# Kernel tuning notes

Measured on AMD Instinct MI355X. Metric: run time of the kernel, lower is better.

## Reference

```python
import jax, jax.numpy as jnp
import numpy as np

EMBED, HEADS, LEVELS, POINTS, CAMS, ZANCH = 256, 8, 4, 8, 6, 4
HEAD_DIM = EMBED // HEADS
NQ, BS = 10000, 1
SHAPES = np.array([[92, 160], [46, 80], [23, 40], [12, 20]], dtype=np.int64)
NV = int((SHAPES[:, 0] * SHAPES[:, 1]).sum())  # 19560


def setup_inputs() -> dict:
    key = jax.random.key(0)
    ks = jax.random.split(key, 10)
    f = lambda k, s, sc=1.0: jax.random.normal(k, s, dtype=jnp.float32) * sc
    lsi = np.concatenate([[0], np.cumsum(SHAPES[:, 0] * SHAPES[:, 1])[:-1]]).astype(np.int64)
    return dict(
        query=f(ks[0], (BS, NQ, EMBED)),
        query_pos=f(ks[1], (BS, NQ, EMBED)),
        value=f(ks[2], (CAMS, NV, BS, EMBED)),
        reference_points=jax.random.uniform(ks[3], (CAMS, BS, NQ, ZANCH, 2), dtype=jnp.float32),
        bev_mask=jax.random.bernoulli(ks[4], 0.3, (CAMS, BS, NQ, ZANCH)),
        spatial_shapes=jnp.asarray(SHAPES),
        level_start_index=jnp.asarray(lsi),
        Wv=f(ks[5], (EMBED, EMBED), 0.02), bv=jnp.zeros((EMBED,), jnp.float32),
        Woff=f(ks[6], (EMBED, HEADS * LEVELS * POINTS * 2), 0.02),
        boff=f(ks[7], (HEADS * LEVELS * POINTS * 2,), 0.5),
        Watt=f(ks[8], (EMBED, HEADS * LEVELS * POINTS), 0.02),
        batt=jnp.zeros((HEADS * LEVELS * POINTS,), jnp.float32),
        Wout=f(ks[9], (EMBED, EMBED), 0.02), bout=jnp.zeros((EMBED,), jnp.float32),
    )


def _bilinear_gather(v2, x, y, H, W):
    # v2: (BH, H*W, hd); x, y: (BH, N) pixel coords. grid_sample bilinear,
    # align_corners=False, padding_mode='zeros' semantics.
    x0 = jnp.floor(x); y0 = jnp.floor(y)
    lx = x - x0; ly = y - y0
    x0i = x0.astype(jnp.int32); y0i = y0.astype(jnp.int32)
    out = jnp.zeros(x.shape + (v2.shape[-1],), v2.dtype)
    for dx, dy, w in ((0, 0, (1 - lx) * (1 - ly)), (1, 0, lx * (1 - ly)),
                      (0, 1, (1 - lx) * ly), (1, 1, lx * ly)):
        xi = x0i + dx; yi = y0i + dy
        valid = (xi >= 0) & (xi < W) & (yi >= 0) & (yi < H)
        idx = jnp.clip(yi, 0, H - 1) * W + jnp.clip(xi, 0, W - 1)
        g = jnp.take_along_axis(v2, idx[..., None], axis=1)
        out = out + g * (w * valid.astype(v2.dtype))[..., None]
    return out


def _ms_deform_attn(q, v, ref, shapes, lsi, Wv, bv, Woff, boff, Watt, batt):
    # q: (B, nq, C); v: (B, nv, C); ref: (B, nq, D, 2)
    B, nq, C = q.shape
    v = (v @ Wv + bv).reshape(B, -1, HEADS, HEAD_DIM)
    off = (q @ Woff + boff).reshape(B, nq, HEADS, LEVELS, POINTS, 2)
    attw = jax.nn.softmax((q @ Watt + batt).reshape(B, nq, HEADS, LEVELS * POINTS), axis=-1)
    attw = attw.reshape(B, nq, HEADS, LEVELS, POINTS)
    # offset normalizer: (w_l, h_l) per level
    norm = jnp.asarray(np.stack([shapes[:, 1], shapes[:, 0]], -1), q.dtype)  # (L, 2)
    off = off / norm[None, None, None, :, None, :]
    off = off.reshape(B, nq, HEADS, LEVELS, POINTS // ZANCH, ZANCH, 2)
    loc = (ref[:, :, None, None, None] + off).reshape(B, nq, HEADS, LEVELS, POINTS, 2)
    acc = jnp.zeros((B, HEADS, nq, HEAD_DIM), q.dtype)
    for l in range(LEVELS):
        H, W = int(shapes[l, 0]), int(shapes[l, 1])
        s = int(lsi[l])
        vl = v[:, s:s + H * W].transpose(0, 2, 1, 3).reshape(B * HEADS, H * W, HEAD_DIM)
        ll = loc[:, :, :, l].transpose(0, 2, 1, 3, 4).reshape(B * HEADS, nq * POINTS, 2)
        x = ll[..., 0] * W - 0.5
        y = ll[..., 1] * H - 0.5
        samp = _bilinear_gather(vl, x, y, H, W).reshape(B, HEADS, nq, POINTS, HEAD_DIM)
        w = attw[:, :, :, l].transpose(0, 2, 1, 3)  # (B, HEADS, nq, POINTS)
        acc = acc + (samp * w[..., None]).sum(3)
    return acc.transpose(0, 2, 1, 3).reshape(B, nq, C)


def reference(query, query_pos, value, reference_points, bev_mask, spatial_shapes,
              level_start_index, Wv, bv, Woff, boff, Watt, batt, Wout, bout):
    shapes = np.asarray(spatial_shapes)
    lsi = np.asarray(level_start_index)
    B, nq, C = query.shape
    cams = value.shape[0]
    q = query + query_pos
    # replicate queries per camera (equivalent to rebatch-by-mask: unselected
    # outputs are masked out before accumulation)
    q_cam = jnp.broadcast_to(q[:, None], (B, cams, nq, C)).reshape(B * cams, nq, C)
    v = value.transpose(2, 0, 1, 3).reshape(B * cams, -1, C)
    ref = reference_points.transpose(1, 0, 2, 3, 4).reshape(B * cams, nq, ZANCH, 2)
    out = _ms_deform_attn(q_cam, v, ref, shapes, lsi, Wv, bv, Woff, boff, Watt, batt)
    out = out.reshape(B, cams, nq, C)
    # query selection per camera uses batch 0 of bev_mask, as in the original
    m = (bev_mask[:, 0].sum(-1) > 0)  # (cams, nq)
    slots = (out * m[None, :, :, None].astype(out.dtype)).sum(1)  # (B, nq, C)
    count = (bev_mask.sum(-1) > 0).astype(query.dtype).transpose(1, 2, 0).sum(-1)
    count = jnp.maximum(count, 1.0)  # (B, nq)
    slots = slots / count[..., None]
    # dropout in eval mode is identity
    return slots @ Wout + bout + query
```

## Files before the change

### kernel.cpp

```cpp
#include <hip/hip_runtime.h>
#include <hip/hip_bf16.h>

constexpr int NQ = 10000, NV = 19560, CAMS = 6, EMBED = 256, HEADS = 8,
              HEAD_DIM = 32, LEVELS = 4, POINTS = 8;
constexpr int MQ_PAD = 10112;
constexpr int MV_PAD = 117376;

typedef unsigned int u32;
typedef unsigned short u16;
typedef unsigned char u8;
typedef __attribute__((ext_vector_type(8))) short short8v;
typedef __attribute__((ext_vector_type(4))) float f32x4;
typedef __attribute__((ext_vector_type(2))) float f32x2;

__device__ inline u16 f2bf(float f) {
  __hip_bfloat16 b = __float2bfloat16(f);
  return *(u16*)&b;
}

__global__ void conv_bf16_kernel(const float* __restrict__ a, const float* __restrict__ b,
                                 u16* __restrict__ dst, int M, int Mpad) {
  int i = blockIdx.x * blockDim.x + threadIdx.x;
  if (i >= Mpad * 32) return;
  int row = i >> 5;
  int col = (i & 31) * 8;
  u16 o[8];
  if (row < M) {
    const float* pa = a + (size_t)row * 256 + col;
#pragma unroll
    for (int j = 0; j < 8; ++j) {
      float v = pa[j];
      if (b) v += b[(size_t)row * 256 + col + j];
      o[j] = f2bf(v);
    }
  } else {
#pragma unroll
    for (int j = 0; j < 8; ++j) o[j] = 0;
  }
  *(short8v*)&dst[(size_t)row * 256 + col] = *(short8v*)o;
}

__global__ void transpose_w_kernel(const float* __restrict__ src, u16* __restrict__ dst, int N) {
  int g = blockIdx.x * blockDim.x + threadIdx.x;
  if (g >= N * 256) return;
  int n = g >> 8, k = g & 255;
  dst[(size_t)n * 256 + k] = f2bf(src[(size_t)k * N + n]);
}

__global__ void catbias_kernel(const float* __restrict__ boff, const float* __restrict__ batt,
                               float* __restrict__ catb) {
  int i = blockIdx.x * blockDim.x + threadIdx.x;
  if (i < 512) catb[i] = boff[i];
  else if (i < 768) catb[i] = batt[i - 512];
}

__global__ void mask_kernel(const int* __restrict__ bev, unsigned char* __restrict__ m,
                            float* __restrict__ cinv) {
  int q = blockIdx.x * blockDim.x + threadIdx.x;
  if (q >= NQ) return;
  int cnt = 0;
  for (int c = 0; c < CAMS; ++c) {
    int any = 0;
    for (int z = 0; z < 4; ++z) any |= bev[((size_t)c * NQ + q) * 4 + z];
    m[c * NQ + q] = (unsigned char)(any != 0);
    cnt += (any != 0);
  }
  cinv[q] = 1.0f / (float)(cnt > 0 ? cnt : 1);
}

__global__ __launch_bounds__(256) void gemm_mfma(
    const u16* __restrict__ A, const u16* __restrict__ Bt,
    const float* __restrict__ bias, const float* __restrict__ add,
    void* __restrict__ Cout, void* __restrict__ Cout2, int M, int N, int mode) {
  constexpr int K = 256, BK = 64;
  __shared__ u16 As[128 * BK];
  __shared__ u16 Bs[128 * BK];
  const int tid = threadIdx.x;
  const int lane = tid & 63, w = tid >> 6;
  const int wr = w >> 1, wc = w & 1;
  const int row0 = blockIdx.y * 128, col0 = blockIdx.x * 128;
  f32x4 acc[4][4] = {};

  for (int k0 = 0; k0 < K; k0 += BK) {
    short8v areg[4], breg[4];
#pragma unroll
    for (int j = 0; j < 4; ++j) {
      int e = tid + j * 256;
      int r = e >> 3, cb = (e & 7) * 16;
      areg[j] = *(const short8v*)((const char*)A + ((size_t)(row0 + r) * K + k0) * 2 + cb);
      breg[j] = *(const short8v*)((const char*)Bt + ((size_t)(col0 + r) * K + k0) * 2 + cb);
    }
    __syncthreads();
#pragma unroll
    for (int j = 0; j < 4; ++j) {
      int e = tid + j * 256;
      int r = e >> 3, cb = (e & 7) * 16;
      int sw = cb ^ ((r & 7) << 4);
      *(short8v*)((char*)As + r * 128 + sw) = areg[j];
      *(short8v*)((char*)Bs + r * 128 + sw) = breg[j];
    }
    __syncthreads();
#pragma unroll
    for (int kk = 0; kk < 2; ++kk) {
      short8v af[4], bf[4];
#pragma unroll
      for (int m = 0; m < 4; ++m) {
        int r = wr * 64 + m * 16 + (lane & 15);
        int cb = kk * 64 + (lane >> 4) * 16;
        af[m] = *(const short8v*)((const char*)As + r * 128 + (cb ^ ((r & 7) << 4)));
      }
#pragma unroll
      for (int n = 0; n < 4; ++n) {
        int r = wc * 64 + n * 16 + (lane & 15);
        int cb = kk * 64 + (lane >> 4) * 16;
        bf[n] = *(const short8v*)((const char*)Bs + r * 128 + (cb ^ ((r & 7) << 4)));
      }
#pragma unroll
      for (int m = 0; m < 4; ++m)
#pragma unroll
        for (int n = 0; n < 4; ++n)
          acc[m][n] = __builtin_amdgcn_mfma_f32_16x16x32_bf16(af[m], bf[n], acc[m][n], 0, 0, 0);
    }
  }

#pragma unroll
  for (int m = 0; m < 4; ++m) {
    int rowb = row0 + wr * 64 + m * 16 + (lane >> 4) * 4;
#pragma unroll
    for (int r = 0; r < 4; ++r) {
      int rr = rowb + r;
      if (rr >= M) continue;
#pragma unroll
      for (int n = 0; n < 4; ++n) {
        int col = col0 + wc * 64 + n * 16 + (lane & 15);
        float v = acc[m][n][r] + bias[col];
        if (mode == 0) {
          ((float*)Cout)[(size_t)rr * N + col] = v;
        } else if (mode == 2) {
          ((float*)Cout)[(size_t)rr * N + col] = v + add[(size_t)rr * N + col];
        } else {
          if (col < 512) ((float*)Cout)[(size_t)rr * 512 + col] = v;
          else           ((float*)Cout2)[(size_t)rr * 256 + (col - 512)] = v;
        }
      }
    }
  }
}

__global__ __launch_bounds__(256) void gemm_wv_f32(
    const float* __restrict__ A, const u16* __restrict__ Bt,
    const float* __restrict__ bias, u8* __restrict__ Cout, int M) {
  constexpr int K = 256, BK = 64, N = 256;
  __shared__ u16 As[128 * BK];
  __shared__ u16 Bs[128 * BK];
  const int tid = threadIdx.x;
  const int lane = tid & 63, w = tid >> 6;
  const int wr = w >> 1, wc = w & 1;
  const int row0 = blockIdx.y * 128, col0 = blockIdx.x * 128;
  f32x4 acc[4][4] = {};

  for (int k0 = 0; k0 < K; k0 += BK) {
    short8v areg[4], breg[4];
#pragma unroll
    for (int j = 0; j < 4; ++j) {
      int e = tid + j * 256;
      int r = e >> 3, co = (e & 7) * 8;
      u16 tmp[8];
      if (row0 + r < M) {
        const float* src = A + (size_t)(row0 + r) * K + k0 + co;
        float4 f0 = *(const float4*)src;
        float4 f1 = *(const float4*)(src + 4);
        tmp[0] = f2bf(f0.x); tmp[1] = f2bf(f0.y); tmp[2] = f2bf(f0.z); tmp[3] = f2bf(f0.w);
        tmp[4] = f2bf(f1.x); tmp[5] = f2bf(f1.y); tmp[6] = f2bf(f1.z); tmp[7] = f2bf(f1.w);
      } else {
#pragma unroll
        for (int t = 0; t < 8; ++t) tmp[t] = 0;
      }
      areg[j] = *(short8v*)tmp;
      breg[j] = *(const short8v*)((const char*)Bt + ((size_t)(col0 + r) * K + k0) * 2 + co * 2);
    }
    __syncthreads();
#pragma unroll
    for (int j = 0; j < 4; ++j) {
      int e = tid + j * 256;
      int r = e >> 3, cb = (e & 7) * 16;
      int sw = cb ^ ((r & 7) << 4);
      *(short8v*)((char*)As + r * 128 + sw) = areg[j];
      *(short8v*)((char*)Bs + r * 128 + sw) = breg[j];
    }
    __syncthreads();
#pragma unroll
    for (int kk = 0; kk < 2; ++kk) {
      short8v af[4], bf[4];
#pragma unroll
      for (int m = 0; m < 4; ++m) {
        int r = wr * 64 + m * 16 + (lane & 15);
        int cb = kk * 64 + (lane >> 4) * 16;
        af[m] = *(const short8v*)((const char*)As + r * 128 + (cb ^ ((r & 7) << 4)));
      }
#pragma unroll
      for (int n = 0; n < 4; ++n) {
        int r = wc * 64 + n * 16 + (lane & 15);
        int cb = kk * 64 + (lane >> 4) * 16;
        bf[n] = *(const short8v*)((const char*)Bs + r * 128 + (cb ^ ((r & 7) << 4)));
      }
#pragma unroll
      for (int m = 0; m < 4; ++m)
#pragma unroll
        for (int n = 0; n < 4; ++n)
          acc[m][n] = __builtin_amdgcn_mfma_f32_16x16x32_bf16(af[m], bf[n], acc[m][n], 0, 0, 0);
    }
  }

#pragma unroll
  for (int m = 0; m < 4; ++m) {
    int rowb = row0 + wr * 64 + m * 16 + (lane >> 4) * 4;
#pragma unroll
    for (int r = 0; r < 4; ++r) {
      int rr = rowb + r;
      if (rr >= M) continue;
      int cam = rr / NV;
      int px = rr - cam * NV;
#pragma unroll
      for (int n = 0; n < 4; ++n) {
        int col = col0 + wc * 64 + n * 16 + (lane & 15);
        float v = acc[m][n][r] + bias[col];
        int h = col >> 5, d = col & 31;
        int pk = __builtin_amdgcn_cvt_pk_fp8_f32(v, v, 0, false);
        Cout[(((size_t)cam * HEADS + h) * NV + px) * 32 + d] = (u8)(pk & 0xff);
      }
    }
  }
}

__global__ void softmax_kernel(float* __restrict__ att) {
  int r = blockIdx.x * blockDim.x + threadIdx.x;
  if (r >= NQ * HEADS) return;
  float* p = att + (size_t)r * 32;
  float mx = -1e30f;
#pragma unroll
  for (int i = 0; i < 32; ++i) mx = fmaxf(mx, p[i]);
  float e[32], sm = 0.f;
#pragma unroll
  for (int i = 0; i < 32; ++i) { e[i] = expf(p[i] - mx); sm += e[i]; }
  float inv = 1.0f / sm;
#pragma unroll
  for (int i = 0; i < 32; ++i) p[i] = e[i] * inv;
}

__global__ __launch_bounds__(256, 8) void sample_kernel(
    const u8* __restrict__ vproj, const float* __restrict__ offr,
    const float* __restrict__ attw, const float* __restrict__ ref,
    const unsigned char* __restrict__ m, float* __restrict__ part) {
  constexpr int Hs[4] = {92, 46, 23, 12};
  constexpr int Ws[4] = {160, 80, 40, 20};
  constexpr int LSI[4] = {0, 14720, 18400, 19320};
  const int c = blockIdx.y;
  const int q = blockIdx.x * 4 + (threadIdx.x >> 6);
  if (!m[c * NQ + q]) return;
  const int lane = threadIdx.x & 63;
  const int h = lane >> 3;
  const int pp = (lane >> 2) & 1;
  const int d0 = (lane & 3) * 8;

  float acc[8] = {};
  const float* refc = ref + ((size_t)c * NQ + q) * 8;
  float rfx[4], rfy[4];
#pragma unroll
  for (int z = 0; z < 4; ++z) { rfx[z] = refc[z * 2]; rfy[z] = refc[z * 2 + 1]; }
  const float* offq = offr + (size_t)q * 512 + h * 64;
  const float* attq = attw + (size_t)q * 256 + h * 32;
  const u8* vch = vproj + ((size_t)c * HEADS + h) * NV * 32 + d0;

#pragma unroll
  for (int l = 0; l < LEVELS; ++l) {
    const int W = Ws[l], H = Hs[l];
    const u8* vl = vch + (size_t)LSI[l] * 32;
#pragma unroll 2
    for (int pi = 0; pi < 4; ++pi) {
      const int p = pi * 2 + pp;
      const int z = p & 3;
      float2 o = *(const float2*)&offq[l * 16 + p * 2];
      float x = rfx[z] * (float)W + o.x - 0.5f;
      float y = rfy[z] * (float)H + o.y - 0.5f;
      float x0f = floorf(x), y0f = floorf(y);
      float lx = x - x0f, ly = y - y0f;
      int x0 = (int)x0f, y0 = (int)y0f;
      float fx0 = (x0 >= 0 && x0 < W) ? 1.f : 0.f;
      float fx1 = (x0 >= -1 && x0 < W - 1) ? 1.f : 0.f;
      float fy0 = (y0 >= 0 && y0 < H) ? 1.f : 0.f;
      float fy1 = (y0 >= -1 && y0 < H - 1) ? 1.f : 0.f;
      int x0c = min(max(x0, 0), W - 1);
      int x1c = min(max(x0 + 1, 0), W - 1);
      int y0c = min(max(y0, 0), H - 1);
      int y1c = min(max(y0 + 1, 0), H - 1);
      uint2 v00 = *(const uint2*)(vl + (size_t)(y0c * W + x0c) * 32);
      uint2 v01 = *(const uint2*)(vl + (size_t)(y0c * W + x1c) * 32);
      uint2 v10 = *(const uint2*)(vl + (size_t)(y1c * W + x0c) * 32);
      uint2 v11 = *(const uint2*)(vl + (size_t)(y1c * W + x1c) * 32);
      float a = attq[l * 8 + p];
      float c00 = a * (1.f - lx) * (1.f - ly) * fx0 * fy0;
      float c01 = a * lx * (1.f - ly) * fx1 * fy0;
      float c10 = a * (1.f - lx) * ly * fx0 * fy1;
      float c11 = a * lx * ly * fx1 * fy1;
#pragma unroll
      for (int half = 0; half < 2; ++half) {
        u32 w00 = half ? v00.y : v00.x, w01 = half ? v01.y : v01.x;
        u32 w10 = half ? v10.y : v10.x, w11 = half ? v11.y : v11.x;
        f32x2 gA0 = __builtin_amdgcn_cvt_pk_f32_fp8(w00, false);
        f32x2 gA1 = __builtin_amdgcn_cvt_pk_f32_fp8(w00, true);
        f32x2 gB0 = __builtin_amdgcn_cvt_pk_f32_fp8(w01, false);
        f32x2 gB1 = __builtin_amdgcn_cvt_pk_f32_fp8(w01, true);
        f32x2 gC0 = __builtin_amdgcn_cvt_pk_f32_fp8(w10, false);
        f32x2 gC1 = __builtin_amdgcn_cvt_pk_f32_fp8(w10, true);
        f32x2 gD0 = __builtin_amdgcn_cvt_pk_f32_fp8(w11, false);
        f32x2 gD1 = __builtin_amdgcn_cvt_pk_f32_fp8(w11, true);
        int b = half * 4;
        acc[b + 0] += c00 * gA0.x + c01 * gB0.x + c10 * gC0.x + c11 * gD0.x;
        acc[b + 1] += c00 * gA0.y + c01 * gB0.y + c10 * gC0.y + c11 * gD0.y;
        acc[b + 2] += c00 * gA1.x + c01 * gB1.x + c10 * gC1.x + c11 * gD1.x;
        acc[b + 3] += c00 * gA1.y + c01 * gB1.y + c10 * gC1.y + c11 * gD1.y;
      }
    }
  }
#pragma unroll
  for (int d = 0; d < 8; ++d) acc[d] += __shfl_xor(acc[d], 4);
  if (pp == 0) {
    float* sp = part + ((size_t)c * NQ + q) * EMBED + h * 32 + d0;
    f32x4 v0 = {acc[0], acc[1], acc[2], acc[3]};
    f32x4 v1 = {acc[4], acc[5], acc[6], acc[7]};
    __builtin_nontemporal_store(v0, (f32x4*)sp);
    __builtin_nontemporal_store(v1, (f32x4*)(sp + 4));
  }
}

__global__ void reduce_kernel(const float* __restrict__ part, const unsigned char* __restrict__ m,
                              const float* __restrict__ cinv, u16* __restrict__ sbf) {
  int i = blockIdx.x * blockDim.x + threadIdx.x;
  if (i >= MQ_PAD * 32) return;
  int row = i >> 5;
  int col = (i & 31) * 8;
  u16 o[8];
  if (row < NQ) {
    float s[8] = {};
    for (int c = 0; c < CAMS; ++c) {
      if (!m[c * NQ + row]) continue;
      const f32x4* pp = (const f32x4*)(part + ((size_t)c * NQ + row) * EMBED + col);
      f32x4 f0 = __builtin_nontemporal_load(pp);
      f32x4 f1 = __builtin_nontemporal_load(pp + 1);
#pragma unroll
      for (int j = 0; j < 4; ++j) { s[j] += f0[j]; s[4 + j] += f1[j]; }
    }
    float sc = cinv[row];
#pragma unroll
    for (int j = 0; j < 8; ++j) o[j] = f2bf(s[j] * sc);
  } else {
#pragma unroll
    for (int j = 0; j < 8; ++j) o[j] = 0;
  }
  *(short8v*)&sbf[(size_t)row * 256 + col] = *(short8v*)o;
}

extern "C" void kernel_launch(void* const* d_in, const int* in_sizes, int n_in,
                              void* d_out, int out_size, void* d_ws, size_t ws_size,
                              hipStream_t stream) {
  const float* query     = (const float*)d_in[0];
  const float* query_pos = (const float*)d_in[1];
  const float* value     = (const float*)d_in[2];
  const float* refpts    = (const float*)d_in[3];
  const int*   bev       = (const int*)d_in[4];
  const float* Wv   = (const float*)d_in[7];
  const float* bv   = (const float*)d_in[8];
  const float* Woff = (const float*)d_in[9];
  const float* boff = (const float*)d_in[10];
  const float* Watt = (const float*)d_in[11];
  const float* batt = (const float*)d_in[12];
  const float* Wout = (const float*)d_in[13];
  const float* bout = (const float*)d_in[14];
  float* out = (float*)d_out;

  char* ws = (char*)d_ws;
  auto alloc = [&](size_t bytes) {
    char* p = ws;
    ws += (bytes + 255) & ~(size_t)255;
    return p;
  };
  u16*   qbf   = (u16*)alloc((size_t)MQ_PAD * 256 * 2);
  u16*   sbf   = (u16*)alloc((size_t)MQ_PAD * 256 * 2);
  u16*   WvT   = (u16*)alloc((size_t)256 * 256 * 2);
  u16*   WqT   = (u16*)alloc((size_t)768 * 256 * 2);
  u16*   WoutT = (u16*)alloc((size_t)256 * 256 * 2);
  float* catb  = (float*)alloc((size_t)768 * 4);
  float* offr  = (float*)alloc((size_t)MQ_PAD * 512 * 4);
  float* attw  = (float*)alloc((size_t)MQ_PAD * 256 * 4);
  u8*    vproj = (u8*)alloc((size_t)CAMS * NV * EMBED);
  float* part  = (float*)alloc((size_t)CAMS * NQ * EMBED * 4);
  float* cinv  = (float*)alloc((size_t)NQ * 4);
  unsigned char* msk = (unsigned char*)alloc((size_t)CAMS * NQ);

  conv_bf16_kernel<<<(MQ_PAD * 32 + 255) / 256, 256, 0, stream>>>(query, query_pos, qbf, NQ, MQ_PAD);
  mask_kernel<<<(NQ + 255) / 256, 256, 0, stream>>>(bev, msk, cinv);
  transpose_w_kernel<<<512, 256, 0, stream>>>(Woff, WqT, 512);
  transpose_w_kernel<<<256, 256, 0, stream>>>(Watt, WqT + (size_t)512 * 256, 256);
  transpose_w_kernel<<<256, 256, 0, stream>>>(Wv, WvT, 256);
  transpose_w_kernel<<<256, 256, 0, stream>>>(Wout, WoutT, 256);
  catbias_kernel<<<3, 256, 0, stream>>>(boff, batt, catb);

  dim3 gQ(768 / 128, MQ_PAD / 128);
  gemm_mfma<<<gQ, 256, 0, stream>>>(qbf, WqT, catb, nullptr, offr, attw, NQ, 768, 3);
  softmax_kernel<<<(NQ * HEADS + 255) / 256, 256, 0, stream>>>(attw);

  dim3 gV(256 / 128, MV_PAD / 128);
  gemm_wv_f32<<<gV, 256, 0, stream>>>(value, WvT, bv, vproj, CAMS * NV);

  dim3 gS(NQ / 4, CAMS);
  sample_kernel<<<gS, 256, 0, stream>>>(vproj, offr, attw, refpts, msk, part);

  reduce_kernel<<<(MQ_PAD * 32 + 255) / 256, 256, 0, stream>>>(part, msk, cinv, sbf);
  dim3 gOut(256 / 128, MQ_PAD / 128);
  gemm_mfma<<<gOut, 256, 0, stream>>>(sbf, WoutT, bout, query, out, nullptr, NQ, 256, 2);
}
```

Measured before the change: 447.9 us.

## Bucket-sort sampling work items by reference point for gather locality

Splits each (camera, query) sampling task into four per-z-anchor work items and sorts them into spatial buckets by reference point using histogram, scan and scatter kernels. Each wavefront in the sample kernel handles one sorted item, so neighbouring waves gather from nearby value pixels and cache reuse should improve. The offset and attention GEMM outputs are permuted to a z-major layout to match, and per-z partial sums are written as bf16 and summed in the reduce kernel. The cost is three extra small kernels with atomics, four times as many partial rows to write and read, and bf16 rounding of partial sums.

```diff
diff --git a/kernel.cpp b/kernel.cpp
--- a/kernel.cpp
+++ b/kernel.cpp
@@ -5,6 +5,8 @@
               HEAD_DIM = 32, LEVELS = 4, POINTS = 8;
 constexpr int MQ_PAD = 10112;
 constexpr int MV_PAD = 117376;
+constexpr int NBUCK = CAMS * 128;
+constexpr int MAXITEMS = CAMS * NQ * 4;
 
 typedef unsigned int u32;
 typedef unsigned short u16;
@@ -17,6 +19,7 @@
   __hip_bfloat16 b = __float2bfloat16(f);
   return *(u16*)&b;
 }
+__device__ inline float bf2f(u16 v) { union { u32 i; float f; } x; x.i = (u32)v << 16; return x.f; }
 
 __global__ void conv_bf16_kernel(const float* __restrict__ a, const float* __restrict__ b,
                                  u16* __restrict__ dst, int M, int Mpad) {
@@ -66,6 +69,57 @@
     cnt += (any != 0);
   }
   cinv[q] = 1.0f / (float)(cnt > 0 ? cnt : 1);
+}
+
+__device__ inline int buck_key(int c, float rx, float ry) {
+  int tx = min(max((int)(rx * 16.f), 0), 15);
+  int ty = min(max((int)(ry * 8.f), 0), 7);
+  return c * 128 + ty * 16 + tx;
+}
+
+__global__ void hist_kernel(const float* __restrict__ ref, const unsigned char* __restrict__ m,
+                            u32* __restrict__ hist) {
+  int q = blockIdx.x * blockDim.x + threadIdx.x;
+  if (q >= NQ) return;
+  for (int c = 0; c < CAMS; ++c) {
+    if (!m[c * NQ + q]) continue;
+    const float* rc = ref + ((size_t)c * NQ + q) * 8;
+#pragma unroll
+    for (int z = 0; z < 4; ++z)
+      atomicAdd(&hist[buck_key(c, rc[z * 2], rc[z * 2 + 1])], 1u);
+  }
+}
+
+__global__ void scan_kernel(const u32* __restrict__ hist, u32* __restrict__ cursor,
+                            u32* __restrict__ total) {
+  __shared__ u32 tmp[NBUCK];
+  int t = threadIdx.x;
+  u32 v = hist[t];
+  tmp[t] = v;
+  __syncthreads();
+  for (int d = 1; d < NBUCK; d <<= 1) {
+    u32 add = (t >= d) ? tmp[t - d] : 0;
+    __syncthreads();
+    tmp[t] += add;
+    __syncthreads();
+  }
+  cursor[t] = tmp[t] - v;
+  if (t == NBUCK - 1) *total = tmp[t];
+}
+
+__global__ void scatter_kernel(const float* __restrict__ ref, const unsigned char* __restrict__ m,
+                               u32* __restrict__ cursor, u32* __restrict__ perm) {
+  int q = blockIdx.x * blockDim.x + threadIdx.x;
+  if (q >= NQ) return;
+  for (int c = 0; c < CAMS; ++c) {
+    if (!m[c * NQ + q]) continue;
+    const float* rc = ref + ((size_t)c * NQ + q) * 8;
+#pragma unroll
+    for (int z = 0; z < 4; ++z) {
+      u32 pos = atomicAdd(&cursor[buck_key(c, rc[z * 2], rc[z * 2 + 1])], 1u);
+      perm[pos] = ((u32)c << 16) | ((u32)z << 14) | (u32)q;
+    }
+  }
 }
 
 __global__ __launch_bounds__(256) void gemm_mfma(
@@ -139,8 +193,16 @@
         } else if (mode == 2) {
           ((float*)Cout)[(size_t)rr * N + col] = v + add[(size_t)rr * N + col];
         } else {
-          if (col < 512) ((float*)Cout)[(size_t)rr * 512 + col] = v;
-          else           ((float*)Cout2)[(size_t)rr * 256 + (col - 512)] = v;
+          if (col < 512) {
+            int h = col >> 6, rem = col & 63, l = rem >> 4, p = (rem >> 1) & 7, xy = col & 1;
+            int z = p & 3, pi = p >> 2;
+            ((float*)Cout)[(size_t)rr * 512 + z * 128 + h * 16 + l * 4 + pi * 2 + xy] = v;
+          } else {
+            int c2 = col - 512;
+            int h = c2 >> 5, rem = c2 & 31, l = rem >> 3, p = rem & 7;
+            int z = p & 3, pi = p >> 2;
+            ((float*)Cout2)[(size_t)rr * 256 + z * 64 + h * 8 + l * 2 + pi] = v;
+          }
         }
       }
     }
@@ -236,105 +298,119 @@
 __global__ void softmax_kernel(float* __restrict__ att) {
   int r = blockIdx.x * blockDim.x + threadIdx.x;
   if (r >= NQ * HEADS) return;
-  float* p = att + (size_t)r * 32;
+  int q = r >> 3, h = r & 7;
+  float* base = att + (size_t)q * 256 + h * 8;
+  float v[32];
   float mx = -1e30f;
-#pragma unroll
-  for (int i = 0; i < 32; ++i) mx = fmaxf(mx, p[i]);
-  float e[32], sm = 0.f;
-#pragma unroll
-  for (int i = 0; i < 32; ++i) { e[i] = expf(p[i] - mx); sm += e[i]; }
+  int n = 0;
+#pragma unroll
+  for (int z = 0; z < 4; ++z)
+#pragma unroll
+    for (int l = 0; l < 4; ++l)
+#pragma unroll
+      for (int pi = 0; pi < 2; ++pi) {
+        float x = base[z * 64 + l * 2 + pi];
+        v[n++] = x;
+        mx = fmaxf(mx, x);
+      }
+  float sm = 0.f;
+#pragma unroll
+  for (int i = 0; i < 32; ++i) { v[i] = expf(v[i] - mx); sm += v[i]; }
   float inv = 1.0f / sm;
-#pragma unroll
-  for (int i = 0; i < 32; ++i) p[i] = e[i] * inv;
+  n = 0;
+#pragma unroll
+  for (int z = 0; z < 4; ++z)
+#pragma unroll
+    for (int l = 0; l < 4; ++l)
+#pragma unroll
+      for (int pi = 0; pi < 2; ++pi)
+        base[z * 64 + l * 2 + pi] = v[n++] * inv;
 }
 
 __global__ __launch_bounds__(256, 8) void sample_kernel(
     const u8* __restrict__ vproj, const float* __restrict__ offr,
     const float* __restrict__ attw, const float* __restrict__ ref,
-    const unsigned char* __restrict__ m, float* __restrict__ part) {
+    const u32* __restrict__ perm, const u32* __restrict__ total,
+    u16* __restrict__ part2) {
   constexpr int Hs[4] = {92, 46, 23, 12};
   constexpr int Ws[4] = {160, 80, 40, 20};
   constexpr int LSI[4] = {0, 14720, 18400, 19320};
-  const int c = blockIdx.y;
-  const int q = blockIdx.x * 4 + (threadIdx.x >> 6);
-  if (!m[c * NQ + q]) return;
+  const int idx = blockIdx.x * 4 + (threadIdx.x >> 6);
+  if (idx >= (int)*total) return;
+  const u32 item = perm[idx];
+  const int c = item >> 16;
+  const int z = (item >> 14) & 3;
+  const int q = item & 0x3fff;
   const int lane = threadIdx.x & 63;
   const int h = lane >> 3;
   const int pp = (lane >> 2) & 1;
   const int d0 = (lane & 3) * 8;
 
+  const float* rc = ref + ((size_t)c * NQ + q) * 8 + z * 2;
+  const float rx = rc[0], ry = rc[1];
+  const float* offq = offr + (size_t)q * 512 + z * 128 + h * 16;
+  const float* attq = attw + (size_t)q * 256 + z * 64 + h * 8;
+  const u8* vch = vproj + ((size_t)c * HEADS + h) * NV * 32 + d0;
+
   float acc[8] = {};
-  const float* refc = ref + ((size_t)c * NQ + q) * 8;
-  float rfx[4], rfy[4];
-#pragma unroll
-  for (int z = 0; z < 4; ++z) { rfx[z] = refc[z * 2]; rfy[z] = refc[z * 2 + 1]; }
-  const float* offq = offr + (size_t)q * 512 + h * 64;
-  const float* attq = attw + (size_t)q * 256 + h * 32;
-  const u8* vch = vproj + ((size_t)c * HEADS + h) * NV * 32 + d0;
-
-#pragma unroll
+#pragma unroll 2
   for (int l = 0; l < LEVELS; ++l) {
     const int W = Ws[l], H = Hs[l];
     const u8* vl = vch + (size_t)LSI[l] * 32;
-#pragma unroll 2
-    for (int pi = 0; pi < 4; ++pi) {
-      const int p = pi * 2 + pp;
-      const int z = p & 3;
-      float2 o = *(const float2*)&offq[l * 16 + p * 2];
-      float x = rfx[z] * (float)W + o.x - 0.5f;
-      float y = rfy[z] * (float)H + o.y - 0.5f;
-      float x0f = floorf(x), y0f = floorf(y);
-      float lx = x - x0f, ly = y - y0f;
-      int x0 = (int)x0f, y0 = (int)y0f;
-      float fx0 = (x0 >= 0 && x0 < W) ? 1.f : 0.f;
-      float fx1 = (x0 >= -1 && x0 < W - 1) ? 1.f : 0.f;
-      float fy0 = (y0 >= 0 && y0 < H) ? 1.f : 0.f;
-      float fy1 = (y0 >= -1 && y0 < H - 1) ? 1.f : 0.f;
-      int x0c = min(max(x0, 0), W - 1);
-      int x1c = min(max(x0 + 1, 0), W - 1);
-      int y0c = min(max(y0, 0), H - 1);
-      int y1c = min(max(y0 + 1, 0), H - 1);
-      uint2 v00 = *(const uint2*)(vl + (size_t)(y0c * W + x0c) * 32);
-      uint2 v01 = *(const uint2*)(vl + (size_t)(y0c * W + x1c) * 32);
-      uint2 v10 = *(const uint2*)(vl + (size_t)(y1c * W + x0c) * 32);
-      uint2 v11 = *(const uint2*)(vl + (size_t)(y1c * W + x1c) * 32);
-      float a = attq[l * 8 + p];
-      float c00 = a * (1.f - lx) * (1.f - ly) * fx0 * fy0;
-      float c01 = a * lx * (1.f - ly) * fx1 * fy0;
-      float c10 = a * (1.f - lx) * ly * fx0 * fy1;
-      float c11 = a * lx * ly * fx1 * fy1;
-#pragma unroll
-      for (int half = 0; half < 2; ++half) {
-        u32 w00 = half ? v00.y : v00.x, w01 = half ? v01.y : v01.x;
-        u32 w10 = half ? v10.y : v10.x, w11 = half ? v11.y : v11.x;
-        f32x2 gA0 = __builtin_amdgcn_cvt_pk_f32_fp8(w00, false);
-        f32x2 gA1 = __builtin_amdgcn_cvt_pk_f32_fp8(w00, true);
-        f32x2 gB0 = __builtin_amdgcn_cvt_pk_f32_fp8(w01, false);
-        f32x2 gB1 = __builtin_amdgcn_cvt_pk_f32_fp8(w01, true);
-        f32x2 gC0 = __builtin_amdgcn_cvt_pk_f32_fp8(w10, false);
-        f32x2 gC1 = __builtin_amdgcn_cvt_pk_f32_fp8(w10, true);
-        f32x2 gD0 = __builtin_amdgcn_cvt_pk_f32_fp8(w11, false);
-        f32x2 gD1 = __builtin_amdgcn_cvt_pk_f32_fp8(w11, true);
-        int b = half * 4;
-        acc[b + 0] += c00 * gA0.x + c01 * gB0.x + c10 * gC0.x + c11 * gD0.x;
-        acc[b + 1] += c00 * gA0.y + c01 * gB0.y + c10 * gC0.y + c11 * gD0.y;
-        acc[b + 2] += c00 * gA1.x + c01 * gB1.x + c10 * gC1.x + c11 * gD1.x;
-        acc[b + 3] += c00 * gA1.y + c01 * gB1.y + c10 * gC1.y + c11 * gD1.y;
-      }
+    float2 o = *(const float2*)&offq[l * 4 + pp * 2];
+    float a = attq[l * 2 + pp];
+    float x = rx * (float)W + o.x - 0.5f;
+    float y = ry * (float)H + o.y - 0.5f;
+    float x0f = floorf(x), y0f = floorf(y);
+    float lx = x - x0f, ly = y - y0f;
+    int x0 = (int)x0f, y0 = (int)y0f;
+    float fx0 = (x0 >= 0 && x0 < W) ? 1.f : 0.f;
+    float fx1 = (x0 >= -1 && x0 < W - 1) ? 1.f : 0.f;
+    float fy0 = (y0 >= 0 && y0 < H) ? 1.f : 0.f;
+    float fy1 = (y0 >= -1 && y0 < H - 1) ? 1.f : 0.f;
+    int x0c = min(max(x0, 0), W - 1);
+    int x1c = min(max(x0 + 1, 0), W - 1);
+    int y0c = min(max(y0, 0), H - 1);
+    int y1c = min(max(y0 + 1, 0), H - 1);
+    uint2 v00 = *(const uint2*)(vl + (size_t)(y0c * W + x0c) * 32);
+    uint2 v01 = *(const uint2*)(vl + (size_t)(y0c * W + x1c) * 32);
+    uint2 v10 = *(const uint2*)(vl + (size_t)(y1c * W + x0c) * 32);
+    uint2 v11 = *(const uint2*)(vl + (size_t)(y1c * W + x1c) * 32);
+    float c00 = a * (1.f - lx) * (1.f - ly) * fx0 * fy0;
+    float c01 = a * lx * (1.f - ly) * fx1 * fy0;
+    float c10 = a * (1.f - lx) * ly * fx0 * fy1;
+    float c11 = a * lx * ly * fx1 * fy1;
+#pragma unroll
+    for (int half = 0; half < 2; ++half) {
+      u32 w00 = half ? v00.y : v00.x, w01 = half ? v01.y : v01.x;
+      u32 w10 = half ? v10.y : v10.x, w11 = half ? v11.y : v11.x;
+      f32x2 gA0 = __builtin_amdgcn_cvt_pk_f32_fp8(w00, false);
+      f32x2 gA1 = __builtin_amdgcn_cvt_pk_f32_fp8(w00, true);
+      f32x2 gB0 = __builtin_amdgcn_cvt_pk_f32_fp8(w01, false);
+      f32x2 gB1 = __builtin_amdgcn_cvt_pk_f32_fp8(w01, true);
+      f32x2 gC0 = __builtin_amdgcn_cvt_pk_f32_fp8(w10, false);
+      f32x2 gC1 = __builtin_amdgcn_cvt_pk_f32_fp8(w10, true);
+      f32x2 gD0 = __builtin_amdgcn_cvt_pk_f32_fp8(w11, false);
+      f32x2 gD1 = __builtin_amdgcn_cvt_pk_f32_fp8(w11, true);
+      int b = half * 4;
+      acc[b + 0] += c00 * gA0.x + c01 * gB0.x + c10 * gC0.x + c11 * gD0.x;
+      acc[b + 1] += c00 * gA0.y + c01 * gB0.y + c10 * gC0.y + c11 * gD0.y;
+      acc[b + 2] += c00 * gA1.x + c01 * gB1.x + c10 * gC1.x + c11 * gD1.x;
+      acc[b + 3] += c00 * gA1.y + c01 * gB1.y + c10 * gC1.y + c11 * gD1.y;
     }
   }
 #pragma unroll
   for (int d = 0; d < 8; ++d) acc[d] += __shfl_xor(acc[d], 4);
   if (pp == 0) {
-    float* sp = part + ((size_t)c * NQ + q) * EMBED + h * 32 + d0;
-    f32x4 v0 = {acc[0], acc[1], acc[2], acc[3]};
-    f32x4 v1 = {acc[4], acc[5], acc[6], acc[7]};
-    __builtin_nontemporal_store(v0, (f32x4*)sp);
-    __builtin_nontemporal_store(v1, (f32x4*)(sp + 4));
-  }
-}
-
-__global__ void reduce_kernel(const float* __restrict__ part, const unsigned char* __restrict__ m,
+    u16 o[8];
+#pragma unroll
+    for (int d = 0; d < 8; ++d) o[d] = f2bf(acc[d]);
+    short8v* sp = (short8v*)&part2[((size_t)(z * CAMS + c) * NQ + q) * EMBED + h * 32 + d0];
+    __builtin_nontemporal_store(*(short8v*)o, sp);
+  }
+}
+
+__global__ void reduce_kernel(const u16* __restrict__ part2, const unsigned char* __restrict__ m,
                               const float* __restrict__ cinv, u16* __restrict__ sbf) {
   int i = blockIdx.x * blockDim.x + threadIdx.x;
   if (i >= MQ_PAD * 32) return;
@@ -345,11 +421,13 @@
     float s[8] = {};
     for (int c = 0; c < CAMS; ++c) {
       if (!m[c * NQ + row]) continue;
-      const f32x4* pp = (const f32x4*)(part + ((size_t)c * NQ + row) * EMBED + col);
-      f32x4 f0 = __builtin_nontemporal_load(pp);
-      f32x4 f1 = __builtin_nontemporal_load(pp + 1);
-#pragma unroll
-      for (int j = 0; j < 4; ++j) { s[j] += f0[j]; s[4 + j] += f1[j]; }
+#pragma unroll
+      for (int z = 0; z < 4; ++z) {
+        const short8v* pp = (const short8v*)&part2[((size_t)(z * CAMS + c) * NQ + row) * EMBED + col];
+        short8v v = __builtin_nontemporal_load(pp);
+#pragma unroll
+        for (int j = 0; j < 8; ++j) s[j] += bf2f((u16)v[j]);
+      }
     }
     float sc = cinv[row];
 #pragma unroll
@@ -394,9 +472,15 @@
   float* offr  = (float*)alloc((size_t)MQ_PAD * 512 * 4);
   float* attw  = (float*)alloc((size_t)MQ_PAD * 256 * 4);
   u8*    vproj = (u8*)alloc((size_t)CAMS * NV * EMBED);
-  float* part  = (float*)alloc((size_t)CAMS * NQ * EMBED * 4);
+  u16*   part2 = (u16*)alloc((size_t)4 * CAMS * NQ * EMBED * 2);
   float* cinv  = (float*)alloc((size_t)NQ * 4);
   unsigned char* msk = (unsigned char*)alloc((size_t)CAMS * NQ);
+  u32*   hist  = (u32*)alloc((size_t)NBUCK * 4);
+  u32*   cursor= (u32*)alloc((size_t)NBUCK * 4);
+  u32*   total = (u32*)alloc(256);
+  u32*   perm  = (u32*)alloc((size_t)MAXITEMS * 4);
+
+  hipMemsetAsync(hist, 0, NBUCK * 4, stream);
 
   conv_bf16_kernel<<<(MQ_PAD * 32 + 255) / 256, 256, 0, stream>>>(query, query_pos, qbf, NQ, MQ_PAD);
   mask_kernel<<<(NQ + 255) / 256, 256, 0, stream>>>(bev, msk, cinv);
@@ -406,6 +490,10 @@
   transpose_w_kernel<<<256, 256, 0, stream>>>(Wout, WoutT, 256);
   catbias_kernel<<<3, 256, 0, stream>>>(boff, batt, catb);
 
+  hist_kernel<<<(NQ + 255) / 256, 256, 0, stream>>>(refpts, msk, hist);
+  scan_kernel<<<1, NBUCK, 0, stream>>>(hist, cursor, total);
+  scatter_kernel<<<(NQ + 255) / 256, 256, 0, stream>>>(refpts, msk, cursor, perm);
+
   dim3 gQ(768 / 128, MQ_PAD / 128);
   gemm_mfma<<<gQ, 256, 0, stream>>>(qbf, WqT, catb, nullptr, offr, attw, NQ, 768, 3);
   softmax_kernel<<<(NQ * HEADS + 255) / 256, 256, 0, stream>>>(attw);
@@ -413,10 +501,9 @@
   dim3 gV(256 / 128, MV_PAD / 128);
   gemm_wv_f32<<<gV, 256, 0, stream>>>(value, WvT, bv, vproj, CAMS * NV);
 
-  dim3 gS(NQ / 4, CAMS);
-  sample_kernel<<<gS, 256, 0, stream>>>(vproj, offr, attw, refpts, msk, part);
-
-  reduce_kernel<<<(MQ_PAD * 32 + 255) / 256, 256, 0, stream>>>(part, msk, cinv, sbf);
+  sample_kernel<<<MAXITEMS / 4, 256, 0, stream>>>(vproj, offr, attw, refpts, perm, total, part2);
+
+  reduce_kernel<<<(MQ_PAD * 32 + 255) / 256, 256, 0, stream>>>(part2, msk, cinv, sbf);
   dim3 gOut(256 / 128, MQ_PAD / 128);
   gemm_mfma<<<gOut, 256, 0, stream>>>(sbf, WoutT, bout, query, out, nullptr, NQ, 256, 2);
 }
```

Measured after the change: 468.4 us. +4.6%, slower.
